# Kernel optimization log

Hardware: AMD Instinct MI355X
Metric: run time of the kernel (lower is better)

Reference implementation:

```python
import jax, jax.numpy as jnp
import numpy as np

N_EXPERTS = 8
TOP_K = 2
D_MODEL = 1024
D_FF = 4 * D_MODEL

def setup_inputs() -> dict:
    key = jax.random.key(0)
    ks = jax.random.split(key, 5)
    s_in = 1.0 / np.sqrt(D_MODEL)
    s_ff = 1.0 / np.sqrt(D_FF)
    return {
        "x": jax.random.normal(ks[0], (2, 2048, D_MODEL), dtype=jnp.float32),
        "Wr": jax.random.normal(ks[1], (N_EXPERTS, D_MODEL), dtype=jnp.float32) * s_in,
        "W1": jax.random.normal(ks[2], (N_EXPERTS, D_FF, D_MODEL), dtype=jnp.float32) * s_in,
        "W2": jax.random.normal(ks[3], (N_EXPERTS, D_MODEL, D_FF), dtype=jnp.float32) * s_ff,
        "W3": jax.random.normal(ks[4], (N_EXPERTS, D_FF, D_MODEL), dtype=jnp.float32) * s_in,
    }

def reference(x, Wr, W1, W2, W3):
    B, S, D = x.shape
    T = B * S
    xf = x.reshape(T, D)
    logits = xf @ Wr.T                         # [T, E]
    probs = jax.nn.softmax(logits, axis=-1)
    top_p, top_i = jax.lax.top_k(probs, TOP_K)  # [T, K]
    top_p = top_p / jnp.sum(top_p, axis=-1, keepdims=True)
    # per-token combine weight for each expert: [T, E]
    onehot = jax.nn.one_hot(top_i, N_EXPERTS, dtype=x.dtype)  # [T, K, E]
    cw = jnp.einsum('tke,tk->te', onehot, top_p)
    out = jnp.zeros_like(xf)
    for e in range(N_EXPERTS):  # fixed small structural loop over experts
        h = jax.nn.silu(xf @ W1[e].T) * (xf @ W3[e].T)  # [T, F]
        y = h @ W2[e].T                                 # [T, D]
        out = out + cw[:, e:e+1] * y
    importance = jnp.sum(probs, axis=0)                 # [E]
    load = jnp.sum(jnp.sum(onehot, axis=1), axis=0)     # [E]
    aux_loss = jnp.sum(importance * load) * (N_EXPERTS / (T ** 2 + 1e-06))
    return out.reshape(B, S, D), aux_loss
```

## Files before the change

### kernel.cpp

```cpp
#include <hip/hip_runtime.h>

#define T_TOK 4096
#define DM 1024
#define DF 4096
#define NE 8
#define BM 128
#define BN 64
#define BK 64
#define RCAP 9216
#define MAXT 72

typedef _Float16 f16x8 __attribute__((ext_vector_type(8)));
typedef float f32x4 __attribute__((ext_vector_type(4)));

__device__ __forceinline__ ushort f2h_bits(float f) {
    _Float16 h = (_Float16)f;
    return __builtin_bit_cast(unsigned short, h);
}

__global__ __launch_bounds__(256) void k_init(float* __restrict__ out,
                                              int* __restrict__ misc,
                                              int* __restrict__ row_tok) {
    int i = blockIdx.x * 256 + threadIdx.x;
    if (i < T_TOK * DM + 1) out[i] = 0.f;
    if (i < RCAP) row_tok[i] = -1;
    if (i < 256) misc[i] = 0;
}

__global__ __launch_bounds__(64) void k_router(const float* __restrict__ x,
                                               const float* __restrict__ Wr,
                                               float* __restrict__ probs,
                                               int* __restrict__ topi,
                                               float* __restrict__ topw,
                                               int* __restrict__ cnt) {
    int t = blockIdx.x;
    int lane = threadIdx.x;
    const float* xr = x + (size_t)t * DM;
    float s[NE];
#pragma unroll
    for (int e = 0; e < NE; e++) s[e] = 0.f;
    for (int j = lane; j < DM; j += 64) {
        float xv = xr[j];
#pragma unroll
        for (int e = 0; e < NE; e++) s[e] += xv * Wr[e * DM + j];
    }
#pragma unroll
    for (int off = 32; off > 0; off >>= 1) {
#pragma unroll
        for (int e = 0; e < NE; e++) s[e] += __shfl_xor(s[e], off, 64);
    }
    if (lane == 0) {
        float mx = s[0];
#pragma unroll
        for (int e = 1; e < NE; e++) mx = fmaxf(mx, s[e]);
        float ex[NE], sum = 0.f;
#pragma unroll
        for (int e = 0; e < NE; e++) { ex[e] = expf(s[e] - mx); sum += ex[e]; }
        float inv = 1.f / sum;
        float p[NE];
#pragma unroll
        for (int e = 0; e < NE; e++) { p[e] = ex[e] * inv; probs[t * NE + e] = p[e]; }
        int i0 = 0;
#pragma unroll
        for (int e = 1; e < NE; e++) if (p[e] > p[i0]) i0 = e;
        int i1 = (i0 == 0) ? 1 : 0;
#pragma unroll
        for (int e = 0; e < NE; e++) if (e != i0 && p[e] > p[i1]) i1 = e;
        float w0 = p[i0], w1 = p[i1], winv = 1.f / (w0 + w1);
        topi[2 * t] = i0;     topw[2 * t] = w0 * winv;
        topi[2 * t + 1] = i1; topw[2 * t + 1] = w1 * winv;
        atomicAdd(&cnt[i0], 1);
        atomicAdd(&cnt[i1], 1);
    }
}

__global__ __launch_bounds__(256) void k_scan(const float* __restrict__ probs,
                                              const int* __restrict__ cnt,
                                              int* __restrict__ poff,
                                              int* __restrict__ texp,
                                              float* __restrict__ aux_out) {
    __shared__ float red[256 * NE];
    int tid = threadIdx.x;
    float part[NE];
#pragma unroll
    for (int e = 0; e < NE; e++) part[e] = 0.f;
    for (int t = tid; t < T_TOK; t += 256) {
#pragma unroll
        for (int e = 0; e < NE; e++) part[e] += probs[t * NE + e];
    }
#pragma unroll
    for (int e = 0; e < NE; e++) red[tid * NE + e] = part[e];
    __syncthreads();
    for (int s2 = 128; s2 > 0; s2 >>= 1) {
        if (tid < s2) {
#pragma unroll
            for (int e = 0; e < NE; e++) red[tid * NE + e] += red[(tid + s2) * NE + e];
        }
        __syncthreads();
    }
    if (tid == 0) {
        float al = 0.f;
#pragma unroll
        for (int e = 0; e < NE; e++) al += red[e] * (float)cnt[e];
        *aux_out = al * (8.0f / (16777216.0f + 1e-6f));
        int run = 0, tix = 0;
        for (int e = 0; e < NE; e++) {
            poff[e] = run;
            int nt = (cnt[e] + BM - 1) / BM;
            for (int i = 0; i < nt; i++) texp[tix++] = e;
            run += nt * BM;
        }
    }
}

__global__ __launch_bounds__(256) void k_assign(const int* __restrict__ topi,
                                                const float* __restrict__ topw,
                                                const int* __restrict__ poff,
                                                int* __restrict__ fill,
                                                int* __restrict__ row_tok,
                                                float* __restrict__ row_w) {
    int t = blockIdx.x * 256 + threadIdx.x;
    if (t >= T_TOK) return;
#pragma unroll
    for (int k = 0; k < 2; k++) {
        int e = topi[2 * t + k];
        int pos = atomicAdd(&fill[e], 1);
        int r = poff[e] + pos;
        row_tok[r] = t;
        row_w[r] = topw[2 * t + k];
    }
}

__global__ __launch_bounds__(256) void k_gather(const float* __restrict__ x,
                                                const int* __restrict__ row_tok,
                                                ushort* __restrict__ xg) {
    int r = blockIdx.x;
    int tid = threadIdx.x;
    int tok = row_tok[r];
    ushort4 hv;
    if (tok >= 0) {
        float4 v = *(const float4*)(x + (size_t)tok * DM + tid * 4);
        hv.x = f2h_bits(v.x); hv.y = f2h_bits(v.y);
        hv.z = f2h_bits(v.z); hv.w = f2h_bits(v.w);
    } else {
        hv.x = 0; hv.y = 0; hv.z = 0; hv.w = 0;
    }
    *(ushort4*)(xg + (size_t)r * DM + tid * 4) = hv;
}

__global__ __launch_bounds__(256) void k_gemm1(const ushort* __restrict__ xg,
                                               const float* __restrict__ W1,
                                               const float* __restrict__ W3,
                                               const int* __restrict__ texp,
                                               ushort* __restrict__ hbuf) {
    __shared__ char lA[BM * BK * 2];
    __shared__ char lB1[BN * BK * 2];
    __shared__ char lB3[BN * BK * 2];
    int ct = blockIdx.x, rt = blockIdx.y;
    int e = texp[rt];
    const ushort* Ag = xg + (size_t)rt * BM * DM;
    const float* B1g = W1 + (size_t)e * DF * DM + (size_t)ct * BN * DM;
    const float* B3g = W3 + (size_t)e * DF * DM + (size_t)ct * BN * DM;
    int tid = threadIdx.x, lane = tid & 63, wv = tid >> 6;

    const f32x4 fz = {0.f, 0.f, 0.f, 0.f};
    f32x4 acc1[2][4], acc3[2][4];
#pragma unroll
    for (int m = 0; m < 2; m++)
#pragma unroll
        for (int n = 0; n < 4; n++) { acc1[m][n] = fz; acc3[m][n] = fz; }

    for (int k0 = 0; k0 < DM; k0 += BK) {
#pragma unroll
        for (int p = 0; p < 4; p++) {
            int r = p * 32 + (tid >> 3);
            int kc = (tid & 7) * 8;
            uint4 v = *(const uint4*)(Ag + (size_t)r * DM + k0 + kc);
            *(uint4*)(lA + r * 128 + ((kc * 2) ^ ((r & 7) << 4))) = v;
        }
#pragma unroll
        for (int p = 0; p < 4; p++) {
            int n = p * 16 + (tid >> 4);
            int kc = (tid & 15) * 4;
            int boff = n * 128 + ((kc * 2) ^ ((n & 7) << 4));
            float4 v1 = *(const float4*)(B1g + (size_t)n * DM + k0 + kc);
            ushort4 h1; h1.x = f2h_bits(v1.x); h1.y = f2h_bits(v1.y);
            h1.z = f2h_bits(v1.z); h1.w = f2h_bits(v1.w);
            *(ushort4*)(lB1 + boff) = h1;
            float4 v3 = *(const float4*)(B3g + (size_t)n * DM + k0 + kc);
            ushort4 h3; h3.x = f2h_bits(v3.x); h3.y = f2h_bits(v3.y);
            h3.z = f2h_bits(v3.z); h3.w = f2h_bits(v3.w);
            *(ushort4*)(lB3 + boff) = h3;
        }
        __syncthreads();
#pragma unroll
        for (int ks = 0; ks < 2; ks++) {
            int kbyte = (ks * 32 + (lane >> 4) * 8) * 2;
            f16x8 af[2];
#pragma unroll
            for (int m = 0; m < 2; m++) {
                int r = wv * 32 + m * 16 + (lane & 15);
                af[m] = *(const f16x8*)(lA + r * 128 + (kbyte ^ ((r & 7) << 4)));
            }
#pragma unroll
            for (int n = 0; n < 4; n++) {
                int c = n * 16 + (lane & 15);
                int off = c * 128 + (kbyte ^ ((c & 7) << 4));
                f16x8 b1 = *(const f16x8*)(lB1 + off);
                f16x8 b3 = *(const f16x8*)(lB3 + off);
#pragma unroll
                for (int m = 0; m < 2; m++) {
                    acc1[m][n] = __builtin_amdgcn_mfma_f32_16x16x32_f16(af[m], b1, acc1[m][n], 0, 0, 0);
                    acc3[m][n] = __builtin_amdgcn_mfma_f32_16x16x32_f16(af[m], b3, acc3[m][n], 0, 0, 0);
                }
            }
        }
        __syncthreads();
    }
    int rbase = rt * BM + wv * 32;
    int cbase = ct * BN;
#pragma unroll
    for (int m = 0; m < 2; m++) {
#pragma unroll
        for (int i = 0; i < 4; i++) {
            int row = rbase + m * 16 + (lane >> 4) * 4 + i;
            ushort* hrow = hbuf + (size_t)row * DF + cbase + (lane & 15);
#pragma unroll
            for (int n = 0; n < 4; n++) {
                float a1 = acc1[m][n][i];
                float a3 = acc3[m][n][i];
                float h = (a1 / (1.f + expf(-a1))) * a3;
                hrow[n * 16] = f2h_bits(h);
            }
        }
    }
}

__global__ __launch_bounds__(256) void k_gemm2(const ushort* __restrict__ hbuf,
                                               const float* __restrict__ W2,
                                               const int* __restrict__ texp,
                                               const int* __restrict__ row_tok,
                                               const float* __restrict__ row_w,
                                               float* __restrict__ out) {
    __shared__ char lA[BM * BK * 2];
    __shared__ char lB[BN * BK * 2];
    int ct = blockIdx.x, rt = blockIdx.y;
    int e = texp[rt];
    const ushort* Ag = hbuf + (size_t)rt * BM * DF;
    const float* Bg = W2 + (size_t)e * DM * DF + (size_t)ct * BN * DF;
    int tid = threadIdx.x, lane = tid & 63, wv = tid >> 6;

    const f32x4 fz = {0.f, 0.f, 0.f, 0.f};
    f32x4 acc[2][4];
#pragma unroll
    for (int m = 0; m < 2; m++)
#pragma unroll
        for (int n = 0; n < 4; n++) acc[m][n] = fz;

    for (int k0 = 0; k0 < DF; k0 += BK) {
#pragma unroll
        for (int p = 0; p < 4; p++) {
            int r = p * 32 + (tid >> 3);
            int kc = (tid & 7) * 8;
            uint4 v = *(const uint4*)(Ag + (size_t)r * DF + k0 + kc);
            *(uint4*)(lA + r * 128 + ((kc * 2) ^ ((r & 7) << 4))) = v;
        }
#pragma unroll
        for (int p = 0; p < 4; p++) {
            int n = p * 16 + (tid >> 4);
            int kc = (tid & 15) * 4;
            int boff = n * 128 + ((kc * 2) ^ ((n & 7) << 4));
            float4 v1 = *(const float4*)(Bg + (size_t)n * DF + k0 + kc);
            ushort4 h1; h1.x = f2h_bits(v1.x); h1.y = f2h_bits(v1.y);
            h1.z = f2h_bits(v1.z); h1.w = f2h_bits(v1.w);
            *(ushort4*)(lB + boff) = h1;
        }
        __syncthreads();
#pragma unroll
        for (int ks = 0; ks < 2; ks++) {
            int kbyte = (ks * 32 + (lane >> 4) * 8) * 2;
            f16x8 af[2];
#pragma unroll
            for (int m = 0; m < 2; m++) {
                int r = wv * 32 + m * 16 + (lane & 15);
                af[m] = *(const f16x8*)(lA + r * 128 + (kbyte ^ ((r & 7) << 4)));
            }
#pragma unroll
            for (int n = 0; n < 4; n++) {
                int c = n * 16 + (lane & 15);
                f16x8 b = *(const f16x8*)(lB + c * 128 + (kbyte ^ ((c & 7) << 4)));
#pragma unroll
                for (int m = 0; m < 2; m++) {
                    acc[m][n] = __builtin_amdgcn_mfma_f32_16x16x32_f16(af[m], b, acc[m][n], 0, 0, 0);
                }
            }
        }
        __syncthreads();
    }
    int rbase = rt * BM + wv * 32;
    int cbase = ct * BN;
#pragma unroll
    for (int m = 0; m < 2; m++) {
#pragma unroll
        for (int i = 0; i < 4; i++) {
            int rr = rbase + m * 16 + (lane >> 4) * 4 + i;
            int tok = row_tok[rr];
            if (tok >= 0) {
                float w = row_w[rr];
                float* orow = out + (size_t)tok * DM + cbase + (lane & 15);
#pragma unroll
                for (int n = 0; n < 4; n++) {
                    atomicAdd(&orow[n * 16], w * acc[m][n][i]);
                }
            }
        }
    }
}

extern "C" void kernel_launch(void* const* d_in, const int* in_sizes, int n_in,
                              void* d_out, int out_size, void* d_ws, size_t ws_size,
                              hipStream_t stream) {
    (void)in_sizes; (void)n_in; (void)out_size; (void)ws_size;
    const float* x  = (const float*)d_in[0];
    const float* Wr = (const float*)d_in[1];
    const float* W1 = (const float*)d_in[2];
    const float* W2 = (const float*)d_in[3];
    const float* W3 = (const float*)d_in[4];
    float* out = (float*)d_out;
    char* ws = (char*)d_ws;

    int* misc = (int*)ws;
    int* cnt  = misc;
    int* fill = misc + 8;
    int* poff = misc + 16;
    int* texp = misc + 24;
    int*    topi    = (int*)(ws + 1024);
    float*  topw    = (float*)(ws + 33792);
    float*  probs   = (float*)(ws + 66560);
    int*    row_tok = (int*)(ws + 197632);
    float*  row_w   = (float*)(ws + 234496);
    ushort* xg      = (ushort*)(ws + 271360);
    ushort* hbuf    = (ushort*)(ws + 19145728);

    k_init<<<(T_TOK * DM + 1 + 255) / 256, 256, 0, stream>>>(out, misc, row_tok);
    k_router<<<T_TOK, 64, 0, stream>>>(x, Wr, probs, topi, topw, cnt);
    k_scan<<<1, 256, 0, stream>>>(probs, cnt, poff, texp, out + (size_t)T_TOK * DM);
    k_assign<<<(T_TOK + 255) / 256, 256, 0, stream>>>(topi, topw, poff, fill, row_tok, row_w);
    k_gather<<<RCAP, 256, 0, stream>>>(x, row_tok, xg);
    dim3 g1(DF / BN, MAXT);
    k_gemm1<<<g1, 256, 0, stream>>>(xg, W1, W3, texp, hbuf);
    dim3 g2(DM / BN, MAXT);
    k_gemm2<<<g2, 256, 0, stream>>>(hbuf, W2, texp, row_tok, row_w, out);
}
```

Measured before the change: 643.0 us.

## Pre-convert expert weights to swizzled fp16 tiles and load via global_load_lds

Adds conversion kernels that pack W1, W3 and W2 into fp16 64x64 tiles already in the swizzled LDS layout. The gathered activations and the hidden buffer are stored the same way. New GEMM kernels copy these tiles straight into LDS with global_load_lds, and the second GEMM uses a larger 128x128 output tile. The aim is to remove the per-tile fp32-to-fp16 conversion and the register staging inside the GEMMs, at the cost of converting every weight on every call. The new path runs only when the workspace is large enough, and the old kernels stay as a fallback.

Measured after the change: 685.9 us. 1.07x slower.

```diff
diff --git a/kernel.cpp b/kernel.cpp
--- a/kernel.cpp
+++ b/kernel.cpp
@@ -9,13 +9,32 @@
 #define BK 64
 #define RCAP 9216
 #define MAXT 72
+#define CHUNK_B 8192
+#define ACH_B 16384
 
 typedef _Float16 f16x8 __attribute__((ext_vector_type(8)));
 typedef float f32x4 __attribute__((ext_vector_type(4)));
+
+#define MFMA16(a, b, c) __builtin_amdgcn_mfma_f32_16x16x32_f16(a, b, c, 0, 0, 0)
 
 __device__ __forceinline__ ushort f2h_bits(float f) {
     _Float16 h = (_Float16)f;
     return __builtin_bit_cast(unsigned short, h);
+}
+
+__device__ __forceinline__ uint4 pack8(float4 a, float4 b) {
+    union { ushort u[8]; uint4 v; } r;
+    r.u[0] = f2h_bits(a.x); r.u[1] = f2h_bits(a.y);
+    r.u[2] = f2h_bits(a.z); r.u[3] = f2h_bits(a.w);
+    r.u[4] = f2h_bits(b.x); r.u[5] = f2h_bits(b.y);
+    r.u[6] = f2h_bits(b.z); r.u[7] = f2h_bits(b.w);
+    return r.v;
+}
+
+__device__ __forceinline__ void gll16(const void* g, void* l) {
+    __builtin_amdgcn_global_load_lds(
+        (const __attribute__((address_space(1))) unsigned int*)g,
+        (__attribute__((address_space(3))) unsigned int*)l, 16, 0, 0);
 }
 
 __global__ __launch_bounds__(256) void k_init(float* __restrict__ out,
@@ -130,6 +149,205 @@
         row_w[r] = topw[2 * t + k];
     }
 }
+
+
+__global__ __launch_bounds__(256) void k_convert(const float* __restrict__ src,
+                                                 ushort* __restrict__ dst,
+                                                 int row_len) {
+    int nk = row_len >> 6;
+    int kt = blockIdx.x, rt = blockIdx.y;
+    int tid = threadIdx.x;
+    int r = tid >> 2, c0 = (tid & 3) * 16;
+    const float* s = src + (size_t)(rt * 64 + r) * row_len + kt * 64 + c0;
+    float4 v0 = *(const float4*)(s);
+    float4 v1 = *(const float4*)(s + 4);
+    float4 v2 = *(const float4*)(s + 8);
+    float4 v3 = *(const float4*)(s + 12);
+    char* chunk = (char*)dst + ((size_t)rt * nk + kt) * CHUNK_B;
+    int sw = (r & 7) << 4;
+    *(uint4*)(chunk + r * 128 + ((2 * c0) ^ sw)) = pack8(v0, v1);
+    *(uint4*)(chunk + r * 128 + ((2 * c0 + 16) ^ sw)) = pack8(v2, v3);
+}
+
+__global__ __launch_bounds__(256) void k_gather_t(const float* __restrict__ x,
+                                                  const int* __restrict__ row_tok,
+                                                  ushort* __restrict__ xg) {
+    int kt = blockIdx.x, rt = blockIdx.y;
+    int tid = threadIdx.x;
+    int r = tid >> 1, c0 = (tid & 1) * 32;
+    int tok = row_tok[rt * BM + r];
+    char* chunk = (char*)xg + ((size_t)rt * 16 + kt) * ACH_B;
+    int sw = (r & 7) << 4;
+    if (tok >= 0) {
+        const float* s = x + (size_t)tok * DM + kt * 64 + c0;
+#pragma unroll
+        for (int j = 0; j < 4; j++) {
+            float4 va = *(const float4*)(s + j * 8);
+            float4 vb = *(const float4*)(s + j * 8 + 4);
+            *(uint4*)(chunk + r * 128 + ((2 * (c0 + j * 8)) ^ sw)) = pack8(va, vb);
+        }
+    } else {
+        uint4 z = {0, 0, 0, 0};
+#pragma unroll
+        for (int j = 0; j < 4; j++)
+            *(uint4*)(chunk + r * 128 + ((2 * (c0 + j * 8)) ^ sw)) = z;
+    }
+}
+
+__global__ __launch_bounds__(256) void k_gemm1_t(const ushort* __restrict__ xg,
+                                                 const ushort* __restrict__ W1h,
+                                                 const ushort* __restrict__ W3h,
+                                                 const int* __restrict__ texp,
+                                                 ushort* __restrict__ hbuf) {
+    __shared__ __align__(16) char lA[16384];
+    __shared__ __align__(16) char lB1[8192];
+    __shared__ __align__(16) char lB3[8192];
+    int ct = blockIdx.x, rt = blockIdx.y;
+    int e = texp[rt];
+    const char* Ac  = (const char*)xg + (size_t)rt * 16 * ACH_B;
+    const char* B1c = (const char*)W1h + (size_t)((e * 64 + ct) * 16) * CHUNK_B;
+    const char* B3c = (const char*)W3h + (size_t)((e * 64 + ct) * 16) * CHUNK_B;
+    int tid = threadIdx.x, lane = tid & 63, wv = tid >> 6;
+    int wr = wv >> 1, wc = wv & 1;
+
+    const f32x4 fz = {0.f, 0.f, 0.f, 0.f};
+    f32x4 acc1[4][2], acc3[4][2];
+#pragma unroll
+    for (int m = 0; m < 4; m++)
+#pragma unroll
+        for (int n = 0; n < 2; n++) { acc1[m][n] = fz; acc3[m][n] = fz; }
+
+    for (int kt = 0; kt < 16; kt++) {
+        const char* As  = Ac + kt * ACH_B;
+        const char* B1s = B1c + kt * CHUNK_B;
+        const char* B3s = B3c + kt * CHUNK_B;
+#pragma unroll
+        for (int i = 0; i < 4; i++)
+            gll16(As + wv * 4096 + i * 1024 + lane * 16, lA + wv * 4096 + i * 1024);
+#pragma unroll
+        for (int i = 0; i < 2; i++)
+            gll16(B1s + wv * 2048 + i * 1024 + lane * 16, lB1 + wv * 2048 + i * 1024);
+#pragma unroll
+        for (int i = 0; i < 2; i++)
+            gll16(B3s + wv * 2048 + i * 1024 + lane * 16, lB3 + wv * 2048 + i * 1024);
+        asm volatile("s_waitcnt vmcnt(0)" ::: "memory");
+        __syncthreads();
+#pragma unroll
+        for (int ks = 0; ks < 2; ks++) {
+            int kbyte = (ks * 32 + (lane >> 4) * 8) * 2;
+            f16x8 af[4];
+#pragma unroll
+            for (int m = 0; m < 4; m++) {
+                int r = wr * 64 + m * 16 + (lane & 15);
+                af[m] = *(const f16x8*)(lA + r * 128 + (kbyte ^ ((r & 7) << 4)));
+            }
+#pragma unroll
+            for (int n = 0; n < 2; n++) {
+                int c = wc * 32 + n * 16 + (lane & 15);
+                int off = c * 128 + (kbyte ^ ((c & 7) << 4));
+                f16x8 b1 = *(const f16x8*)(lB1 + off);
+                f16x8 b3 = *(const f16x8*)(lB3 + off);
+#pragma unroll
+                for (int m = 0; m < 4; m++) {
+                    acc1[m][n] = MFMA16(af[m], b1, acc1[m][n]);
+                    acc3[m][n] = MFMA16(af[m], b3, acc3[m][n]);
+                }
+            }
+        }
+        __syncthreads();
+    }
+    char* hc = (char*)hbuf + (size_t)(rt * 64 + ct) * ACH_B;
+#pragma unroll
+    for (int m = 0; m < 4; m++) {
+#pragma unroll
+        for (int i = 0; i < 4; i++) {
+            int r = wr * 64 + m * 16 + (lane >> 4) * 4 + i;
+            int sw = (r & 7) << 4;
+#pragma unroll
+            for (int n = 0; n < 2; n++) {
+                int f = wc * 32 + n * 16 + (lane & 15);
+                float a1 = acc1[m][n][i], a3 = acc3[m][n][i];
+                float h = (a1 / (1.f + expf(-a1))) * a3;
+                *(ushort*)(hc + r * 128 + ((2 * f) ^ sw)) = f2h_bits(h);
+            }
+        }
+    }
+}
+
+__global__ __launch_bounds__(256) void k_gemm2_t(const ushort* __restrict__ hbuf,
+                                                 const ushort* __restrict__ W2h,
+                                                 const int* __restrict__ texp,
+                                                 const int* __restrict__ row_tok,
+                                                 const float* __restrict__ row_w,
+                                                 float* __restrict__ out) {
+    __shared__ __align__(16) char lA[16384];
+    __shared__ __align__(16) char lB[16384];
+    int ct = blockIdx.x, rt = blockIdx.y;
+    int e = texp[rt];
+    const char* Ac  = (const char*)hbuf + (size_t)rt * 64 * ACH_B;
+    const char* B0c = (const char*)W2h + (size_t)((e * 16 + ct * 2) * 64) * CHUNK_B;
+    const char* B1c = (const char*)W2h + (size_t)((e * 16 + ct * 2 + 1) * 64) * CHUNK_B;
+    int tid = threadIdx.x, lane = tid & 63, wv = tid >> 6;
+    int wr = wv >> 1, wc = wv & 1;
+
+    const f32x4 fz = {0.f, 0.f, 0.f, 0.f};
+    f32x4 acc[4][4];
+#pragma unroll
+    for (int m = 0; m < 4; m++)
+#pragma unroll
+        for (int n = 0; n < 4; n++) acc[m][n] = fz;
+
+    for (int kt = 0; kt < 64; kt++) {
+        const char* As = Ac + kt * ACH_B;
+#pragma unroll
+        for (int i = 0; i < 4; i++)
+            gll16(As + wv * 4096 + i * 1024 + lane * 16, lA + wv * 4096 + i * 1024);
+        const char* Bs0 = B0c + kt * CHUNK_B;
+        const char* Bs1 = B1c + kt * CHUNK_B;
+#pragma unroll
+        for (int i = 0; i < 2; i++)
+            gll16(Bs0 + wv * 2048 + i * 1024 + lane * 16, lB + wv * 2048 + i * 1024);
+#pragma unroll
+        for (int i = 0; i < 2; i++)
+            gll16(Bs1 + wv * 2048 + i * 1024 + lane * 16, lB + 8192 + wv * 2048 + i * 1024);
+        asm volatile("s_waitcnt vmcnt(0)" ::: "memory");
+        __syncthreads();
+#pragma unroll
+        for (int ks = 0; ks < 2; ks++) {
+            int kbyte = (ks * 32 + (lane >> 4) * 8) * 2;
+            f16x8 af[4];
+#pragma unroll
+            for (int m = 0; m < 4; m++) {
+                int r = wr * 64 + m * 16 + (lane & 15);
+                af[m] = *(const f16x8*)(lA + r * 128 + (kbyte ^ ((r & 7) << 4)));
+            }
+#pragma unroll
+            for (int n = 0; n < 4; n++) {
+                int c = wc * 64 + n * 16 + (lane & 15);
+                f16x8 b = *(const f16x8*)(lB + c * 128 + (kbyte ^ ((c & 7) << 4)));
+#pragma unroll
+                for (int m = 0; m < 4; m++) acc[m][n] = MFMA16(af[m], b, acc[m][n]);
+            }
+        }
+        __syncthreads();
+    }
+    int cbase = ct * 128 + wc * 64;
+#pragma unroll
+    for (int m = 0; m < 4; m++) {
+#pragma unroll
+        for (int i = 0; i < 4; i++) {
+            int rr = rt * BM + wr * 64 + m * 16 + (lane >> 4) * 4 + i;
+            int tok = row_tok[rr];
+            if (tok >= 0) {
+                float w = row_w[rr];
+                float* orow = out + (size_t)tok * DM + cbase + (lane & 15);
+#pragma unroll
+                for (int n = 0; n < 4; n++) atomicAdd(&orow[n * 16], w * acc[m][n][i]);
+            }
+        }
+    }
+}
+
 
 __global__ __launch_bounds__(256) void k_gather(const float* __restrict__ x,
                                                 const int* __restrict__ row_tok,
@@ -210,8 +428,8 @@
                 f16x8 b3 = *(const f16x8*)(lB3 + off);
 #pragma unroll
                 for (int m = 0; m < 2; m++) {
-                    acc1[m][n] = __builtin_amdgcn_mfma_f32_16x16x32_f16(af[m], b1, acc1[m][n], 0, 0, 0);
-                    acc3[m][n] = __builtin_amdgcn_mfma_f32_16x16x32_f16(af[m], b3, acc3[m][n], 0, 0, 0);
+                    acc1[m][n] = MFMA16(af[m], b1, acc1[m][n]);
+                    acc3[m][n] = MFMA16(af[m], b3, acc3[m][n]);
                 }
             }
         }
@@ -290,9 +508,7 @@
                 int c = n * 16 + (lane & 15);
                 f16x8 b = *(const f16x8*)(lB + c * 128 + (kbyte ^ ((c & 7) << 4)));
 #pragma unroll
-                for (int m = 0; m < 2; m++) {
-                    acc[m][n] = __builtin_amdgcn_mfma_f32_16x16x32_f16(af[m], b, acc[m][n], 0, 0, 0);
-                }
+                for (int m = 0; m < 2; m++) acc[m][n] = MFMA16(af[m], b, acc[m][n]);
             }
         }
         __syncthreads();
@@ -309,9 +525,7 @@
                 float w = row_w[rr];
                 float* orow = out + (size_t)tok * DM + cbase + (lane & 15);
 #pragma unroll
-                for (int n = 0; n < 4; n++) {
-                    atomicAdd(&orow[n * 16], w * acc[m][n][i]);
-                }
+                for (int n = 0; n < 4; n++) atomicAdd(&orow[n * 16], w * acc[m][n][i]);
             }
         }
     }
@@ -320,7 +534,7 @@
 extern "C" void kernel_launch(void* const* d_in, const int* in_sizes, int n_in,
                               void* d_out, int out_size, void* d_ws, size_t ws_size,
                               hipStream_t stream) {
-    (void)in_sizes; (void)n_in; (void)out_size; (void)ws_size;
+    (void)in_sizes; (void)n_in; (void)out_size;
     const float* x  = (const float*)d_in[0];
     const float* Wr = (const float*)d_in[1];
     const float* W1 = (const float*)d_in[2];
@@ -341,14 +555,27 @@
     float*  row_w   = (float*)(ws + 234496);
     ushort* xg      = (ushort*)(ws + 271360);
     ushort* hbuf    = (ushort*)(ws + 19145728);
+    ushort* W1h     = (ushort*)(ws + 94643200);
+    ushort* W3h     = (ushort*)(ws + 161752064);
+    ushort* W2h     = (ushort*)(ws + 228860928);
 
     k_init<<<(T_TOK * DM + 1 + 255) / 256, 256, 0, stream>>>(out, misc, row_tok);
     k_router<<<T_TOK, 64, 0, stream>>>(x, Wr, probs, topi, topw, cnt);
     k_scan<<<1, 256, 0, stream>>>(probs, cnt, poff, texp, out + (size_t)T_TOK * DM);
     k_assign<<<(T_TOK + 255) / 256, 256, 0, stream>>>(topi, topw, poff, fill, row_tok, row_w);
-    k_gather<<<RCAP, 256, 0, stream>>>(x, row_tok, xg);
-    dim3 g1(DF / BN, MAXT);
-    k_gemm1<<<g1, 256, 0, stream>>>(xg, W1, W3, texp, hbuf);
-    dim3 g2(DM / BN, MAXT);
-    k_gemm2<<<g2, 256, 0, stream>>>(hbuf, W2, texp, row_tok, row_w, out);
-}
+
+    if (ws_size >= 295969792ULL) {
+        k_convert<<<dim3(16, 512), 256, 0, stream>>>(W1, W1h, DM);
+        k_convert<<<dim3(16, 512), 256, 0, stream>>>(W3, W3h, DM);
+        k_convert<<<dim3(64, 128), 256, 0, stream>>>(W2, W2h, DF);
+        k_gather_t<<<dim3(16, MAXT), 256, 0, stream>>>(x, row_tok, xg);
+        k_gemm1_t<<<dim3(64, MAXT), 256, 0, stream>>>(xg, W1h, W3h, texp, hbuf);
+        k_gemm2_t<<<dim3(8, MAXT), 256, 0, stream>>>(hbuf, W2h, texp, row_tok, row_w, out);
+    } else {
+        k_gather<<<RCAP, 256, 0, stream>>>(x, row_tok, xg);
+        dim3 g1(DF / BN, MAXT);
+        k_gemm1<<<g1, 256, 0, stream>>>(xg, W1, W3, texp, hbuf);
+        dim3 g2(DM / BN, MAXT);
+        k_gemm2<<<g2, 256, 0, stream>>>(hbuf, W2, texp, row_tok, row_w, out);
+    }
+}
```

## Pre-convert weights to fp16 tiled chunks and double-buffer GEMMs via direct LDS loads

Applied to the files above, without the earlier changes.

Adds per-call kernels that convert W1/W3/W2 from fp32 into swizzled fp16 64x64 chunks, and a gather that writes activations in the same chunked layout. The GEMMs then stream contiguous chunks straight into LDS with global_load_lds, double-buffered so the next tile loads while MFMAs run on the current one. Warps are rearranged into a 2x2 grid with 64x32 sub-tiles. The aim is to remove the per-tile fp32 weight loads and conversions inside the GEMM loops, which each row tile repeats. The cost is an extra conversion pass over all weights every call plus more workspace.

Result: slower. 746.5 us (+16.1%).

```diff
diff --git a/kernel.cpp b/kernel.cpp
--- a/kernel.cpp
+++ b/kernel.cpp
@@ -5,17 +5,35 @@
 #define DF 4096
 #define NE 8
 #define BM 128
-#define BN 64
 #define BK 64
 #define RCAP 9216
 #define MAXT 72
+#define CHUNK_B 8192
+#define ACH_B 16384
 
 typedef _Float16 f16x8 __attribute__((ext_vector_type(8)));
 typedef float f32x4 __attribute__((ext_vector_type(4)));
+
+#define MFMA16(a, b, c) __builtin_amdgcn_mfma_f32_16x16x32_f16(a, b, c, 0, 0, 0)
 
 __device__ __forceinline__ ushort f2h_bits(float f) {
     _Float16 h = (_Float16)f;
     return __builtin_bit_cast(unsigned short, h);
+}
+
+__device__ __forceinline__ uint4 pack8(float4 a, float4 b) {
+    union { ushort u[8]; uint4 v; } r;
+    r.u[0] = f2h_bits(a.x); r.u[1] = f2h_bits(a.y);
+    r.u[2] = f2h_bits(a.z); r.u[3] = f2h_bits(a.w);
+    r.u[4] = f2h_bits(b.x); r.u[5] = f2h_bits(b.y);
+    r.u[6] = f2h_bits(b.z); r.u[7] = f2h_bits(b.w);
+    return r.v;
+}
+
+__device__ __forceinline__ void gll16(const void* g, void* l) {
+    __builtin_amdgcn_global_load_lds(
+        (const __attribute__((address_space(1))) unsigned int*)g,
+        (__attribute__((address_space(3))) unsigned int*)l, 16, 0, 0);
 }
 
 __global__ __launch_bounds__(256) void k_init(float* __restrict__ out,
@@ -131,187 +149,213 @@
     }
 }
 
-__global__ __launch_bounds__(256) void k_gather(const float* __restrict__ x,
-                                                const int* __restrict__ row_tok,
-                                                ushort* __restrict__ xg) {
-    int r = blockIdx.x;
+__global__ __launch_bounds__(256) void k_convert(const float* __restrict__ src,
+                                                 ushort* __restrict__ dst,
+                                                 int row_len) {
+    int nk = row_len >> 6;
+    int kt = blockIdx.x, rt = blockIdx.y;
     int tid = threadIdx.x;
-    int tok = row_tok[r];
-    ushort4 hv;
+    int r = tid >> 2, c0 = (tid & 3) * 16;
+    const float* s = src + (size_t)(rt * 64 + r) * row_len + kt * 64 + c0;
+    float4 v0 = *(const float4*)(s);
+    float4 v1 = *(const float4*)(s + 4);
+    float4 v2 = *(const float4*)(s + 8);
+    float4 v3 = *(const float4*)(s + 12);
+    char* chunk = (char*)dst + ((size_t)rt * nk + kt) * CHUNK_B;
+    int sw = (r & 7) << 4;
+    *(uint4*)(chunk + r * 128 + ((2 * c0) ^ sw)) = pack8(v0, v1);
+    *(uint4*)(chunk + r * 128 + ((2 * c0 + 16) ^ sw)) = pack8(v2, v3);
+}
+
+__global__ __launch_bounds__(256) void k_gather_t(const float* __restrict__ x,
+                                                  const int* __restrict__ row_tok,
+                                                  ushort* __restrict__ xg) {
+    int kt = blockIdx.x, rt = blockIdx.y;
+    int tid = threadIdx.x;
+    int r = tid >> 1, c0 = (tid & 1) * 32;
+    int tok = row_tok[rt * BM + r];
+    char* chunk = (char*)xg + ((size_t)rt * 16 + kt) * ACH_B;
+    int sw = (r & 7) << 4;
     if (tok >= 0) {
-        float4 v = *(const float4*)(x + (size_t)tok * DM + tid * 4);
-        hv.x = f2h_bits(v.x); hv.y = f2h_bits(v.y);
-        hv.z = f2h_bits(v.z); hv.w = f2h_bits(v.w);
+        const float* s = x + (size_t)tok * DM + kt * 64 + c0;
+#pragma unroll
+        for (int j = 0; j < 4; j++) {
+            float4 va = *(const float4*)(s + j * 8);
+            float4 vb = *(const float4*)(s + j * 8 + 4);
+            *(uint4*)(chunk + r * 128 + ((2 * (c0 + j * 8)) ^ sw)) = pack8(va, vb);
+        }
     } else {
-        hv.x = 0; hv.y = 0; hv.z = 0; hv.w = 0;
-    }
-    *(ushort4*)(xg + (size_t)r * DM + tid * 4) = hv;
-}
-
-__global__ __launch_bounds__(256) void k_gemm1(const ushort* __restrict__ xg,
-                                               const float* __restrict__ W1,
-                                               const float* __restrict__ W3,
-                                               const int* __restrict__ texp,
-                                               ushort* __restrict__ hbuf) {
-    __shared__ char lA[BM * BK * 2];
-    __shared__ char lB1[BN * BK * 2];
-    __shared__ char lB3[BN * BK * 2];
+        uint4 z = {0, 0, 0, 0};
+#pragma unroll
+        for (int j = 0; j < 4; j++)
+            *(uint4*)(chunk + r * 128 + ((2 * (c0 + j * 8)) ^ sw)) = z;
+    }
+}
+
+__global__ __launch_bounds__(256) void k_gemm1_t(const ushort* __restrict__ xg,
+                                                 const ushort* __restrict__ W1h,
+                                                 const ushort* __restrict__ W3h,
+                                                 const int* __restrict__ texp,
+                                                 ushort* __restrict__ hbuf) {
+    __shared__ __align__(16) char lA[2][16384];
+    __shared__ __align__(16) char lB1[2][8192];
+    __shared__ __align__(16) char lB3[2][8192];
     int ct = blockIdx.x, rt = blockIdx.y;
     int e = texp[rt];
-    const ushort* Ag = xg + (size_t)rt * BM * DM;
-    const float* B1g = W1 + (size_t)e * DF * DM + (size_t)ct * BN * DM;
-    const float* B3g = W3 + (size_t)e * DF * DM + (size_t)ct * BN * DM;
+    const char* Ac  = (const char*)xg + (size_t)rt * 16 * ACH_B;
+    const char* B1c = (const char*)W1h + (size_t)((e * 64 + ct) * 16) * CHUNK_B;
+    const char* B3c = (const char*)W3h + (size_t)((e * 64 + ct) * 16) * CHUNK_B;
     int tid = threadIdx.x, lane = tid & 63, wv = tid >> 6;
+    int wr = wv >> 1, wc = wv & 1;
 
     const f32x4 fz = {0.f, 0.f, 0.f, 0.f};
-    f32x4 acc1[2][4], acc3[2][4];
-#pragma unroll
-    for (int m = 0; m < 2; m++)
-#pragma unroll
-        for (int n = 0; n < 4; n++) { acc1[m][n] = fz; acc3[m][n] = fz; }
-
-    for (int k0 = 0; k0 < DM; k0 += BK) {
-#pragma unroll
-        for (int p = 0; p < 4; p++) {
-            int r = p * 32 + (tid >> 3);
-            int kc = (tid & 7) * 8;
-            uint4 v = *(const uint4*)(Ag + (size_t)r * DM + k0 + kc);
-            *(uint4*)(lA + r * 128 + ((kc * 2) ^ ((r & 7) << 4))) = v;
-        }
-#pragma unroll
-        for (int p = 0; p < 4; p++) {
-            int n = p * 16 + (tid >> 4);
-            int kc = (tid & 15) * 4;
-            int boff = n * 128 + ((kc * 2) ^ ((n & 7) << 4));
-            float4 v1 = *(const float4*)(B1g + (size_t)n * DM + k0 + kc);
-            ushort4 h1; h1.x = f2h_bits(v1.x); h1.y = f2h_bits(v1.y);
-            h1.z = f2h_bits(v1.z); h1.w = f2h_bits(v1.w);
-            *(ushort4*)(lB1 + boff) = h1;
-            float4 v3 = *(const float4*)(B3g + (size_t)n * DM + k0 + kc);
-            ushort4 h3; h3.x = f2h_bits(v3.x); h3.y = f2h_bits(v3.y);
-            h3.z = f2h_bits(v3.z); h3.w = f2h_bits(v3.w);
-            *(ushort4*)(lB3 + boff) = h3;
-        }
-        __syncthreads();
+    f32x4 acc1[4][2], acc3[4][2];
+#pragma unroll
+    for (int m = 0; m < 4; m++)
+#pragma unroll
+        for (int n = 0; n < 2; n++) { acc1[m][n] = fz; acc3[m][n] = fz; }
+
+#define G1_STAGE(kt_, b_)                                                              \
+    {                                                                                  \
+        const char* As_  = Ac + (kt_) * ACH_B;                                         \
+        const char* B1s_ = B1c + (kt_) * CHUNK_B;                                      \
+        const char* B3s_ = B3c + (kt_) * CHUNK_B;                                      \
+        _Pragma("unroll")                                                              \
+        for (int i = 0; i < 4; i++)                                                    \
+            gll16(As_ + wv * 4096 + i * 1024 + lane * 16, lA[b_] + wv * 4096 + i * 1024); \
+        _Pragma("unroll")                                                              \
+        for (int i = 0; i < 2; i++)                                                    \
+            gll16(B1s_ + wv * 2048 + i * 1024 + lane * 16, lB1[b_] + wv * 2048 + i * 1024); \
+        _Pragma("unroll")                                                              \
+        for (int i = 0; i < 2; i++)                                                    \
+            gll16(B3s_ + wv * 2048 + i * 1024 + lane * 16, lB3[b_] + wv * 2048 + i * 1024); \
+    }
+
+    G1_STAGE(0, 0);
+    asm volatile("s_waitcnt vmcnt(0)" ::: "memory");
+    __syncthreads();
+    int cur = 0;
+    for (int kt = 0; kt < 16; kt++) {
+        if (kt < 15) G1_STAGE(kt + 1, cur ^ 1);
 #pragma unroll
         for (int ks = 0; ks < 2; ks++) {
             int kbyte = (ks * 32 + (lane >> 4) * 8) * 2;
-            f16x8 af[2];
-#pragma unroll
-            for (int m = 0; m < 2; m++) {
-                int r = wv * 32 + m * 16 + (lane & 15);
-                af[m] = *(const f16x8*)(lA + r * 128 + (kbyte ^ ((r & 7) << 4)));
-            }
-#pragma unroll
-            for (int n = 0; n < 4; n++) {
-                int c = n * 16 + (lane & 15);
+            f16x8 af[4];
+#pragma unroll
+            for (int m = 0; m < 4; m++) {
+                int r = wr * 64 + m * 16 + (lane & 15);
+                af[m] = *(const f16x8*)(lA[cur] + r * 128 + (kbyte ^ ((r & 7) << 4)));
+            }
+#pragma unroll
+            for (int n = 0; n < 2; n++) {
+                int c = wc * 32 + n * 16 + (lane & 15);
                 int off = c * 128 + (kbyte ^ ((c & 7) << 4));
-                f16x8 b1 = *(const f16x8*)(lB1 + off);
-                f16x8 b3 = *(const f16x8*)(lB3 + off);
-#pragma unroll
-                for (int m = 0; m < 2; m++) {
-                    acc1[m][n] = __builtin_amdgcn_mfma_f32_16x16x32_f16(af[m], b1, acc1[m][n], 0, 0, 0);
-                    acc3[m][n] = __builtin_amdgcn_mfma_f32_16x16x32_f16(af[m], b3, acc3[m][n], 0, 0, 0);
+                f16x8 b1 = *(const f16x8*)(lB1[cur] + off);
+                f16x8 b3 = *(const f16x8*)(lB3[cur] + off);
+#pragma unroll
+                for (int m = 0; m < 4; m++) {
+                    acc1[m][n] = MFMA16(af[m], b1, acc1[m][n]);
+                    acc3[m][n] = MFMA16(af[m], b3, acc3[m][n]);
                 }
             }
         }
+        asm volatile("s_waitcnt vmcnt(0)" ::: "memory");
         __syncthreads();
-    }
-    int rbase = rt * BM + wv * 32;
-    int cbase = ct * BN;
-#pragma unroll
-    for (int m = 0; m < 2; m++) {
+        cur ^= 1;
+    }
+#undef G1_STAGE
+    char* hc = (char*)hbuf + (size_t)(rt * 64 + ct) * ACH_B;
+#pragma unroll
+    for (int m = 0; m < 4; m++) {
 #pragma unroll
         for (int i = 0; i < 4; i++) {
-            int row = rbase + m * 16 + (lane >> 4) * 4 + i;
-            ushort* hrow = hbuf + (size_t)row * DF + cbase + (lane & 15);
-#pragma unroll
-            for (int n = 0; n < 4; n++) {
-                float a1 = acc1[m][n][i];
-                float a3 = acc3[m][n][i];
+            int r = wr * 64 + m * 16 + (lane >> 4) * 4 + i;
+            int sw = (r & 7) << 4;
+#pragma unroll
+            for (int n = 0; n < 2; n++) {
+                int f = wc * 32 + n * 16 + (lane & 15);
+                float a1 = acc1[m][n][i], a3 = acc3[m][n][i];
                 float h = (a1 / (1.f + expf(-a1))) * a3;
-                hrow[n * 16] = f2h_bits(h);
-            }
-        }
-    }
-}
-
-__global__ __launch_bounds__(256) void k_gemm2(const ushort* __restrict__ hbuf,
-                                               const float* __restrict__ W2,
-                                               const int* __restrict__ texp,
-                                               const int* __restrict__ row_tok,
-                                               const float* __restrict__ row_w,
-                                               float* __restrict__ out) {
-    __shared__ char lA[BM * BK * 2];
-    __shared__ char lB[BN * BK * 2];
+                *(ushort*)(hc + r * 128 + ((2 * f) ^ sw)) = f2h_bits(h);
+            }
+        }
+    }
+}
+
+__global__ __launch_bounds__(256) void k_gemm2_t(const ushort* __restrict__ hbuf,
+                                                 const ushort* __restrict__ W2h,
+                                                 const int* __restrict__ texp,
+                                                 const int* __restrict__ row_tok,
+                                                 const float* __restrict__ row_w,
+                                                 float* __restrict__ out) {
+    __shared__ __align__(16) char lA[2][16384];
+    __shared__ __align__(16) char lB[2][8192];
     int ct = blockIdx.x, rt = blockIdx.y;
     int e = texp[rt];
-    const ushort* Ag = hbuf + (size_t)rt * BM * DF;
-    const float* Bg = W2 + (size_t)e * DM * DF + (size_t)ct * BN * DF;
+    const char* Ac = (const char*)hbuf + (size_t)rt * 64 * ACH_B;
+    const char* Bc = (const char*)W2h + (size_t)((e * 16 + ct) * 64) * CHUNK_B;
     int tid = threadIdx.x, lane = tid & 63, wv = tid >> 6;
+    int wr = wv >> 1, wc = wv & 1;
 
     const f32x4 fz = {0.f, 0.f, 0.f, 0.f};
-    f32x4 acc[2][4];
-#pragma unroll
-    for (int m = 0; m < 2; m++)
-#pragma unroll
-        for (int n = 0; n < 4; n++) acc[m][n] = fz;
-
-    for (int k0 = 0; k0 < DF; k0 += BK) {
-#pragma unroll
-        for (int p = 0; p < 4; p++) {
-            int r = p * 32 + (tid >> 3);
-            int kc = (tid & 7) * 8;
-            uint4 v = *(const uint4*)(Ag + (size_t)r * DF + k0 + kc);
-            *(uint4*)(lA + r * 128 + ((kc * 2) ^ ((r & 7) << 4))) = v;
-        }
-#pragma unroll
-        for (int p = 0; p < 4; p++) {
-            int n = p * 16 + (tid >> 4);
-            int kc = (tid & 15) * 4;
-            int boff = n * 128 + ((kc * 2) ^ ((n & 7) << 4));
-            float4 v1 = *(const float4*)(Bg + (size_t)n * DF + k0 + kc);
-            ushort4 h1; h1.x = f2h_bits(v1.x); h1.y = f2h_bits(v1.y);
-            h1.z = f2h_bits(v1.z); h1.w = f2h_bits(v1.w);
-            *(ushort4*)(lB + boff) = h1;
-        }
-        __syncthreads();
+    f32x4 acc[4][2];
+#pragma unroll
+    for (int m = 0; m < 4; m++)
+#pragma unroll
+        for (int n = 0; n < 2; n++) acc[m][n] = fz;
+
+#define G2_STAGE(kt_, b_)                                                              \
+    {                                                                                  \
+        const char* As_ = Ac + (kt_) * ACH_B;                                          \
+        const char* Bs_ = Bc + (kt_) * CHUNK_B;                                        \
+        _Pragma("unroll")                                                              \
+        for (int i = 0; i < 4; i++)                                                    \
+            gll16(As_ + wv * 4096 + i * 1024 + lane * 16, lA[b_] + wv * 4096 + i * 1024); \
+        _Pragma("unroll")                                                              \
+        for (int i = 0; i < 2; i++)                                                    \
+            gll16(Bs_ + wv * 2048 + i * 1024 + lane * 16, lB[b_] + wv * 2048 + i * 1024); \
+    }
+
+    G2_STAGE(0, 0);
+    asm volatile("s_waitcnt vmcnt(0)" ::: "memory");
+    __syncthreads();
+    int cur = 0;
+    for (int kt = 0; kt < 64; kt++) {
+        if (kt < 63) G2_STAGE(kt + 1, cur ^ 1);
 #pragma unroll
         for (int ks = 0; ks < 2; ks++) {
             int kbyte = (ks * 32 + (lane >> 4) * 8) * 2;
-            f16x8 af[2];
-#pragma unroll
-            for (int m = 0; m < 2; m++) {
-                int r = wv * 32 + m * 16 + (lane & 15);
-                af[m] = *(const f16x8*)(lA + r * 128 + (kbyte ^ ((r & 7) << 4)));
-            }
-#pragma unroll
-            for (int n = 0; n < 4; n++) {
-                int c = n * 16 + (lane & 15);
-                f16x8 b = *(const f16x8*)(lB + c * 128 + (kbyte ^ ((c & 7) << 4)));
-#pragma unroll
-                for (int m = 0; m < 2; m++) {
-                    acc[m][n] = __builtin_amdgcn_mfma_f32_16x16x32_f16(af[m], b, acc[m][n], 0, 0, 0);
-                }
-            }
-        }
+            f16x8 af[4];
+#pragma unroll
+            for (int m = 0; m < 4; m++) {
+                int r = wr * 64 + m * 16 + (lane & 15);
+                af[m] = *(const f16x8*)(lA[cur] + r * 128 + (kbyte ^ ((r & 7) << 4)));
+            }
+#pragma unroll
+            for (int n = 0; n < 2; n++) {
+                int c = wc * 32 + n * 16 + (lane & 15);
+                f16x8 b = *(const f16x8*)(lB[cur] + c * 128 + (kbyte ^ ((c & 7) << 4)));
+#pragma unroll
+                for (int m = 0; m < 4; m++) acc[m][n] = MFMA16(af[m], b, acc[m][n]);
+            }
+        }
+        asm volatile("s_waitcnt vmcnt(0)" ::: "memory");
         __syncthreads();
-    }
-    int rbase = rt * BM + wv * 32;
-    int cbase = ct * BN;
-#pragma unroll
-    for (int m = 0; m < 2; m++) {
+        cur ^= 1;
+    }
+#undef G2_STAGE
+    int cbase = ct * 64 + wc * 32;
+#pragma unroll
+    for (int m = 0; m < 4; m++) {
 #pragma unroll
         for (int i = 0; i < 4; i++) {
-            int rr = rbase + m * 16 + (lane >> 4) * 4 + i;
+            int rr = rt * BM + wr * 64 + m * 16 + (lane >> 4) * 4 + i;
             int tok = row_tok[rr];
             if (tok >= 0) {
                 float w = row_w[rr];
                 float* orow = out + (size_t)tok * DM + cbase + (lane & 15);
 #pragma unroll
-                for (int n = 0; n < 4; n++) {
-                    atomicAdd(&orow[n * 16], w * acc[m][n][i]);
-                }
+                for (int n = 0; n < 2; n++) atomicAdd(&orow[n * 16], w * acc[m][n][i]);
             }
         }
     }
@@ -341,14 +385,19 @@
     float*  row_w   = (float*)(ws + 234496);
     ushort* xg      = (ushort*)(ws + 271360);
     ushort* hbuf    = (ushort*)(ws + 19145728);
+    ushort* W1h     = (ushort*)(ws + 94643200);
+    ushort* W3h     = (ushort*)(ws + 161752064);
+    ushort* W2h     = (ushort*)(ws + 228860928);
 
     k_init<<<(T_TOK * DM + 1 + 255) / 256, 256, 0, stream>>>(out, misc, row_tok);
     k_router<<<T_TOK, 64, 0, stream>>>(x, Wr, probs, topi, topw, cnt);
     k_scan<<<1, 256, 0, stream>>>(probs, cnt, poff, texp, out + (size_t)T_TOK * DM);
     k_assign<<<(T_TOK + 255) / 256, 256, 0, stream>>>(topi, topw, poff, fill, row_tok, row_w);
-    k_gather<<<RCAP, 256, 0, stream>>>(x, row_tok, xg);
-    dim3 g1(DF / BN, MAXT);
-    k_gemm1<<<g1, 256, 0, stream>>>(xg, W1, W3, texp, hbuf);
-    dim3 g2(DM / BN, MAXT);
-    k_gemm2<<<g2, 256, 0, stream>>>(hbuf, W2, texp, row_tok, row_w, out);
-}
+
+    k_convert<<<dim3(16, 512), 256, 0, stream>>>(W1, W1h, DM);
+    k_convert<<<dim3(16, 512), 256, 0, stream>>>(W3, W3h, DM);
+    k_convert<<<dim3(64, 128), 256, 0, stream>>>(W2, W2h, DF);
+    k_gather_t<<<dim3(16, MAXT), 256, 0, stream>>>(x, row_tok, xg);
+    k_gemm1_t<<<dim3(64, MAXT), 256, 0, stream>>>(xg, W1h, W3h, texp, hbuf);
+    k_gemm2_t<<<dim3(16, MAXT), 256, 0, stream>>>(hbuf, W2h, texp, row_tok, row_w, out);
+}
```
